# Kernel optimization log

Measured on AMD Instinct MI355X. Metric: run time of the kernel, lower is better.

Reference implementation:

```python
import jax, jax.numpy as jnp
import numpy as np

EPS = 1e-7
CAPS_N = 1152   # 32 maps * 6 * 6
CAPS1_DIM = 8
CAPS2_N = 10
CAPS2_DIM = 16


def squash(s, axis):
    sq = jnp.sum(jnp.square(s), axis=axis, keepdims=True)
    norm = jnp.sqrt(sq + EPS)
    return (sq / (1.0 + sq)) * (s / norm)


def _conv(x, k, b, stride):
    y = jax.lax.conv_general_dilated(x, k, (stride, stride), 'VALID',
                                     dimension_numbers=('NHWC', 'HWIO', 'NHWC'))
    return jax.nn.relu(y + b)


def setup_inputs() -> dict:
    key = jax.random.key(0)
    ks = jax.random.split(key, 8)
    B = 256
    return {
        'image': jax.random.uniform(ks[0], (B, 28, 28, 1), dtype=jnp.float32),
        'target': jax.random.randint(ks[1], (B,), 0, CAPS2_N),
        'conv1_w': jax.random.normal(ks[2], (9, 9, 1, 256), jnp.float32) * 0.05,
        'conv1_b': jnp.zeros((256,), jnp.float32),
        'conv2_w': jax.random.normal(ks[3], (9, 9, 256, 256), jnp.float32) * 0.02,
        'conv2_b': jnp.zeros((256,), jnp.float32),
        'W': jax.random.normal(ks[4], (1, CAPS_N, CAPS2_N, CAPS2_DIM, CAPS1_DIM), jnp.float32) * 0.1,
        'd1_w': jax.random.normal(ks[5], (CAPS2_N * CAPS2_DIM, 512), jnp.float32) * 0.05,
        'd1_b': jnp.zeros((512,), jnp.float32),
        'd2_w': jax.random.normal(ks[6], (512, 1024), jnp.float32) * 0.04,
        'd2_b': jnp.zeros((1024,), jnp.float32),
        'd3_w': jax.random.normal(ks[7], (1024, 784), jnp.float32) * 0.03,
        'd3_b': jnp.zeros((784,), jnp.float32),
    }


def reference(image, target, conv1_w, conv1_b, conv2_w, conv2_b, W,
              d1_w, d1_b, d2_w, d2_b, d3_w, d3_b):
    B = image.shape[0]
    h = _conv(image, conv1_w, conv1_b, 1)        # [B,20,20,256]
    h = _conv(h, conv2_w, conv2_b, 2)            # [B,6,6,256]
    pc = squash(h.reshape(B, CAPS_N, CAPS1_DIM), axis=-1)  # [B,1152,8]
    # u_hat[b,n,c,j] = sum_i W[0,n,c,j,i] * pc[b,n,i]  (avoids explicit tiling)
    u_hat = jnp.einsum('ncji,bni->bncj', W[0], pc)          # [B,1152,10,16]
    # round 1: softmax of zeros over the 10 digit caps == uniform 1/10
    s1 = jnp.sum(u_hat, axis=1) * (1.0 / CAPS2_N)           # [B,10,16]
    v1 = squash(s1, axis=-1)
    # agreement uv[b,n,c] = <u_hat[b,n,c,:], v1[b,c,:]>
    uv = jnp.einsum('bncj,bcj->bnc', u_hat, v1)             # [B,1152,10]
    # round 2
    c2 = jax.nn.softmax(uv, axis=2)
    s2 = jnp.einsum('bnc,bncj->bcj', c2, u_hat)             # [B,10,16]
    v2 = squash(s2, axis=-1)                                # [B,10,16]
    norm_v2 = jnp.sqrt(jnp.sum(jnp.square(v2), axis=-1, keepdims=True) + EPS)
    norm_v2 = norm_v2[:, None, :, :, None]                  # [B,1,10,1,1]
    y_pred = jnp.squeeze(jnp.argmax(norm_v2, axis=2), axis=(1, 2))  # [B,1]
    # training path: mask by target one-hot
    mask = jax.nn.one_hot(target, CAPS2_N, dtype=v2.dtype)  # [B,10]
    masked = v2 * mask[:, :, None]                          # [B,10,16]
    flat = masked.reshape(B, 1, CAPS2_N * CAPS2_DIM)        # [B,1,160]
    h1 = jax.nn.relu(flat @ d1_w + d1_b)
    h2 = jax.nn.relu(h1 @ d2_w + d2_b)
    dec = jax.nn.sigmoid(h2 @ d3_w + d3_b)                  # [B,1,784]
    return norm_v2, y_pred, dec
```

## Files before the change

kernel.cpp:

```cpp
#include <hip/hip_runtime.h>
#include <math.h>

#define EPS 1e-7f
#define IN1_ELEMS 26214400
#define BT_ELEMS  5308416

typedef float fvec4 __attribute__((ext_vector_type(4)));
typedef short short8 __attribute__((ext_vector_type(8)));
typedef _Float16 half8 __attribute__((ext_vector_type(8)));

__device__ inline unsigned short f2h(float f){
  _Float16 h = (_Float16)f;
  return __builtin_bit_cast(unsigned short, h);
}
__device__ inline float h2f(unsigned short u){
  return (float)__builtin_bit_cast(_Float16, u);
}
__device__ inline void async16(unsigned short* dst, const unsigned short* src){
  __builtin_amdgcn_global_load_lds((const __attribute__((address_space(1))) void*)src,
                                   (__attribute__((address_space(3))) void*)dst, 16, 0, 0);
}
__device__ inline fvec4 mfma_f16(short8 a, short8 b, fvec4 c){
  return __builtin_amdgcn_mfma_f32_16x16x32_f16(
      __builtin_bit_cast(half8, a), __builtin_bit_cast(half8, b), c, 0, 0, 0);
}

__global__ __launch_bounds__(256) void wt_kernel(const float* __restrict__ w2,
    unsigned short* __restrict__ BTh, unsigned short* __restrict__ BTl,
    float* __restrict__ c2out){
  __shared__ float tile[64][65];
  int t = threadIdx.x;
  int k0 = blockIdx.x * 64, oc0 = blockIdx.y * 64;
  int bid = blockIdx.y*324 + blockIdx.x;
  for (int g = bid*256 + t; g < 2359296; g += 1296*256) c2out[g] = 0.f;
  #pragma unroll
  for (int p = 0; p < 16; ++p){
    int f = p*256 + t;
    int kr = f >> 6, cc = f & 63;
    tile[kr][cc] = w2[(size_t)(k0 + kr)*256 + oc0 + cc];
  }
  __syncthreads();
  #pragma unroll
  for (int p = 0; p < 16; ++p){
    int f = p*256 + t;
    int ocr = f >> 6, kc = f & 63;
    float v = tile[kc][ocr] * 64.f;
    unsigned short h = f2h(v);
    size_t idx = (size_t)(oc0 + ocr)*20736 + k0 + kc;
    BTh[idx] = h;
    BTl[idx] = f2h(v - h2f(h));
  }
}

__global__ __launch_bounds__(256) void conv1_kernel(const float* __restrict__ img,
    const float* __restrict__ w1, const float* __restrict__ b1,
    unsigned short* __restrict__ outh){
  __shared__ float sim[252];
  int t = threadIdx.x;
  int oh = blockIdx.x, b = blockIdx.y;
  if (t < 252) sim[t] = img[((size_t)b*28 + oh + t/28)*28 + (t%28)];
  __syncthreads();
  float acc[20];
  #pragma unroll
  for (int i = 0; i < 20; ++i) acc[i] = 0.f;
  #pragma unroll
  for (int kh = 0; kh < 9; ++kh){
    float im[28];
    #pragma unroll
    for (int c = 0; c < 28; ++c) im[c] = sim[kh*28 + c];
    #pragma unroll
    for (int kw = 0; kw < 9; ++kw){
      float wv = w1[(kh*9 + kw)*256 + t];
      #pragma unroll
      for (int ow = 0; ow < 20; ++ow) acc[ow] = fmaf(im[ow + kw], wv, acc[ow]);
    }
  }
  float bv = b1[t];
  size_t base = ((size_t)(b*20 + oh))*20*256 + t;
  #pragma unroll
  for (int ow = 0; ow < 20; ++ow){
    float v = fmaxf(acc[ow] + bv, 0.f);
    outh[base + ow*256] = f2h(v * 0.015625f);
  }
}

__global__ __launch_bounds__(256) void conv2_mfma(const unsigned short* __restrict__ in1h,
    const unsigned short* __restrict__ BTh, float* __restrict__ out){
  __shared__ __align__(16) unsigned short lds[24576];
  const int t = threadIdx.x;
  const int lane = t & 63, w = t >> 6;
  const int m0 = blockIdx.y * 128, n0 = blockIdx.x * 128;
  const int rowA = t >> 2, q = (t & 3) ^ ((t >> 3) & 3);

  const unsigned short* aS[2];
  const unsigned short* bS[2];
  #pragma unroll
  for (int h = 0; h < 2; ++h){
    int m = m0 + h*64 + rowA;
    int bb = m / 36, s = m - bb*36, oh = s / 6, ow = s - oh*6;
    aS[h] = in1h + ((size_t)((bb*20 + 2*oh)*20 + 2*ow))*256 + q*8;
    int n = n0 + h*64 + rowA;
    bS[h] = BTh + (size_t)n*20736 + q*8;
  }

  const int r = lane & 15;
  const int p = (lane >> 4) ^ ((lane >> 1) & 3);
  int roA[4], roB[4];
  #pragma unroll
  for (int i=0;i<4;++i){
    roA[i] = ((w >> 1)*64 + i*16 + r)*32 + p*8;
    roB[i] = ((w & 1)*64  + i*16 + r)*32 + p*8;
  }

  fvec4 acc[4][4];
  #pragma unroll
  for (int i=0;i<4;++i)
    #pragma unroll
    for (int j=0;j<4;++j) acc[i][j] = (fvec4){0.f,0.f,0.f,0.f};

  const int ks0 = blockIdx.z * 81;

  #define STAGE(BUF, KS) do{                                            \
    int kk_ = (KS) >> 3, kh_ = kk_/9, kw_ = kk_ - kh_*9;                \
    int aoff_ = (kh_*20 + kw_)*256 + ((KS) & 7)*32;                     \
    int boff_ = (KS)*32;                                                \
    int base_ = (BUF)*12288;                                            \
    _Pragma("unroll")                                                   \
    for (int h_=0; h_<2; ++h_){                                         \
      async16(&lds[base_ +        h_*2048 + t*8], aS[h_] + aoff_);      \
      async16(&lds[base_ + 4096 + h_*2048 + t*8], bS[h_] + boff_);      \
      async16(&lds[base_ + 8192 + h_*2048 + t*8], bS[h_] + BT_ELEMS + boff_); \
    } }while(0)

  STAGE(0, ks0);
  int buf = 0;
  for (int it = 0; it < 81; ++it){
    __syncthreads();
    if (it < 80) STAGE(buf^1, ks0 + it + 1);
    int base = buf*12288;
    short8 af[4], bh[4], bl[4];
    #pragma unroll
    for (int i=0;i<4;++i){
      af[i] = *(const short8*)&lds[base + roA[i]];
      bh[i] = *(const short8*)&lds[base + 4096 + roB[i]];
      bl[i] = *(const short8*)&lds[base + 8192 + roB[i]];
    }
    #pragma unroll
    for (int i=0;i<4;++i)
      #pragma unroll
      for (int j=0;j<4;++j){
        acc[i][j] = mfma_f16(af[i], bh[j], acc[i][j]);
        acc[i][j] = mfma_f16(af[i], bl[j], acc[i][j]);
      }
    buf ^= 1;
  }

  const int qm = (w >> 1)*64, qn = (w & 1)*64;
  #pragma unroll
  for (int i=0;i<4;++i){
    int gm = m0 + qm + i*16 + ((lane >> 4) << 2);
    #pragma unroll
    for (int j=0;j<4;++j){
      int gn = n0 + qn + j*16 + (lane & 15);
      #pragma unroll
      for (int rr=0;rr<4;++rr)
        atomicAdd(&out[(size_t)(gm + rr)*256 + gn], acc[i][j][rr]);
    }
  }
}

__global__ __launch_bounds__(256) void squash_pc_kernel(const float* __restrict__ c2out,
    const float* __restrict__ b2, float* __restrict__ pc, float* __restrict__ s1s2){
  int g = blockIdx.x*256 + threadIdx.x;
  if (g < 81920) s1s2[g] = 0.f;
  const float* s = c2out + (size_t)g*8;
  int oc0 = (g & 31) * 8;
  float v[8], sq = 0.f;
  #pragma unroll
  for (int e=0;e<8;++e){ float x = fmaxf(s[e] + b2[oc0+e], 0.f); v[e] = x; sq += x*x; }
  float fac = sq / ((1.f + sq) * sqrtf(sq + EPS));
  float* o = pc + (size_t)g*8;
  #pragma unroll
  for (int e=0;e<8;++e) o[e] = v[e]*fac;
}

__global__ __launch_bounds__(256) void s1_producer(const float* __restrict__ pc,
    const float* __restrict__ Wm, float* __restrict__ s1){
  __shared__ float pcl[2048];
  int t = threadIdx.x;
  int n0 = blockIdx.x * 16, b0 = blockIdx.y * 16;
  #pragma unroll
  for (int p = 0; p < 8; ++p){
    int f = p*256 + t;
    int bl = f >> 7, rem = f & 127;
    pcl[f] = pc[((size_t)(b0 + bl)*1152 + n0)*8 + rem];
  }
  __syncthreads();
  for (int r = 0; r < 10; ++r){
    int item = r*256 + t;
    int bl = item / 160, cj = item - bl*160;
    float s1a = 0.f;
    const float* pb = &pcl[bl*128];
    #pragma unroll 4
    for (int nl = 0; nl < 16; ++nl){
      const float4* wp = (const float4*)&Wm[((size_t)(n0 + nl)*160 + cj)*8];
      float4 w0 = wp[0], w1 = wp[1];
      const float4* pp = (const float4*)&pb[nl*8];
      float4 p0 = pp[0], p1 = pp[1];
      s1a += w0.x*p0.x + w0.y*p0.y + w0.z*p0.z + w0.w*p0.w
           + w1.x*p1.x + w1.y*p1.y + w1.z*p1.z + w1.w*p1.w;
    }
    atomicAdd(&s1[(b0 + bl)*160 + cj], s1a);
  }
}

__global__ __launch_bounds__(320) void routing2(const float* __restrict__ pc,
    const float* __restrict__ Wm, const float* __restrict__ s1, float* __restrict__ s2){
  __shared__ float pcl[32][64];
  __shared__ float v1l[8][160];
  __shared__ float facl[80];
  __shared__ float c2l[32][10][8];
  const int t = threadIdx.x;
  const int n0 = blockIdx.x*32, b0 = blockIdx.y*8;

  for (int f = t; f < 2048; f += 320){
    int b = f >> 8, rem = f & 255;
    pcl[rem >> 3][b*8 + (rem & 7)] =
        pc[((size_t)(b0 + b)*1152 + n0 + (rem >> 3))*8 + (rem & 7)];
  }
  if (t < 80){
    int b = t/10, c = t - (t/10)*10;
    const float* s = s1 + (size_t)(b0 + b)*160 + c*16;
    float sq = 0.f;
    #pragma unroll
    for (int j=0;j<16;++j){ float v = s[j]*0.1f; sq += v*v; }
    facl[t] = 0.1f * sq / ((1.f + sq) * sqrtf(sq + EPS));
  }
  __syncthreads();
  for (int f = t; f < 1280; f += 320){
    int b = f / 160, cj = f - b*160;
    v1l[b][cj] = s1[(size_t)(b0 + b)*160 + cj] * facl[b*10 + (cj >> 4)];
  }
  __syncthreads();

  {
    const int nl = t / 10, c = t - (t/10)*10;
    float pcr[64];
    #pragma unroll
    for (int u = 0; u < 16; ++u) ((float4*)pcr)[u] = ((const float4*)&pcl[nl][0])[u];
    const float* wrow = Wm + ((size_t)(n0 + nl)*160 + c*16)*8;
    float uv[8];
    #pragma unroll
    for (int b=0;b<8;++b) uv[b] = 0.f;
    #pragma unroll
    for (int j = 0; j < 16; ++j){
      float4 w0 = ((const float4*)wrow)[j*2], w1 = ((const float4*)wrow)[j*2+1];
      #pragma unroll
      for (int b=0;b<8;++b){
        float tj = w0.x*pcr[b*8+0] + w0.y*pcr[b*8+1] + w0.z*pcr[b*8+2] + w0.w*pcr[b*8+3]
                 + w1.x*pcr[b*8+4] + w1.y*pcr[b*8+5] + w1.z*pcr[b*8+6] + w1.w*pcr[b*8+7];
        uv[b] = fmaf(tj, v1l[b][c*16 + j], uv[b]);
      }
    }
    #pragma unroll
    for (int b=0;b<8;++b) c2l[nl][c][b] = uv[b];
  }
  __syncthreads();

  if (t < 256){
    int snl = t >> 3, sb = t & 7;
    float mx = c2l[snl][0][sb];
    #pragma unroll
    for (int cc=1;cc<10;++cc) mx = fmaxf(mx, c2l[snl][cc][sb]);
    float e[10], sum = 0.f;
    #pragma unroll
    for (int cc=0;cc<10;++cc){ e[cc] = expf(c2l[snl][cc][sb] - mx); sum += e[cc]; }
    float inv = 1.f/sum;
    #pragma unroll
    for (int cc=0;cc<10;++cc) c2l[snl][cc][sb] = e[cc]*inv;
  }
  __syncthreads();

  {
    const int g = t / 160, cj = t - g*160;
    const int c = cj >> 4;
    float acc0 = 0.f, acc1 = 0.f, acc2 = 0.f, acc3 = 0.f;
    for (int nl = 0; nl < 32; ++nl){
      const float4* wp = (const float4*)&Wm[((size_t)(n0 + nl)*160 + cj)*8];
      float4 w0 = wp[0], w1 = wp[1];
      const float* pb = &pcl[nl][g*32];
      const float* cc = &c2l[nl][c][g*4];
      float4 p0, p1;
      p0 = ((const float4*)pb)[0]; p1 = ((const float4*)pb)[1];
      acc0 = fmaf(cc[0], w0.x*p0.x + w0.y*p0.y + w0.z*p0.z + w0.w*p0.w
                       + w1.x*p1.x + w1.y*p1.y + w1.z*p1.z + w1.w*p1.w, acc0);
      p0 = ((const float4*)pb)[2]; p1 = ((const float4*)pb)[3];
      acc1 = fmaf(cc[1], w0.x*p0.x + w0.y*p0.y + w0.z*p0.z + w0.w*p0.w
                       + w1.x*p1.x + w1.y*p1.y + w1.z*p1.z + w1.w*p1.w, acc1);
      p0 = ((const float4*)pb)[4]; p1 = ((const float4*)pb)[5];
      acc2 = fmaf(cc[2], w0.x*p0.x + w0.y*p0.y + w0.z*p0.z + w0.w*p0.w
                       + w1.x*p1.x + w1.y*p1.y + w1.z*p1.z + w1.w*p1.w, acc2);
      p0 = ((const float4*)pb)[6]; p1 = ((const float4*)pb)[7];
      acc3 = fmaf(cc[3], w0.x*p0.x + w0.y*p0.y + w0.z*p0.z + w0.w*p0.w
                       + w1.x*p1.x + w1.y*p1.y + w1.z*p1.z + w1.w*p1.w, acc3);
    }
    atomicAdd(&s2[(size_t)(b0 + g*4 + 0)*160 + cj], acc0);
    atomicAdd(&s2[(size_t)(b0 + g*4 + 1)*160 + cj], acc1);
    atomicAdd(&s2[(size_t)(b0 + g*4 + 2)*160 + cj], acc2);
    atomicAdd(&s2[(size_t)(b0 + g*4 + 3)*160 + cj], acc3);
  }
}

__global__ __launch_bounds__(64) void finalize_kernel(const float* __restrict__ s2,
    const int* __restrict__ target, float* __restrict__ out_norm,
    float* __restrict__ out_pred, float* __restrict__ masked){
  __shared__ float v2l[160];
  __shared__ float nrm[10];
  int b = blockIdx.x, t = threadIdx.x;
  if (t < 10){
    const float* s = s2 + b*160 + t*16;
    float x[16], sq = 0.f;
    #pragma unroll
    for (int j=0;j<16;++j){ x[j] = s[j]; sq += x[j]*x[j]; }
    float fac = sq / ((1.f + sq) * sqrtf(sq + EPS));
    float n2 = 0.f;
    #pragma unroll
    for (int j=0;j<16;++j){ float v = x[j]*fac; v2l[t*16+j] = v; n2 += v*v; }
    float nr = sqrtf(n2 + EPS);
    nrm[t] = nr;
    out_norm[b*10 + t] = nr;
  }
  __syncthreads();
  if (t == 0){
    int am = 0; float bv = nrm[0];
    #pragma unroll
    for (int c=1;c<10;++c) if (nrm[c] > bv){ bv = nrm[c]; am = c; }
    out_pred[b] = (float)am;
  }
  int tg = target[b];
  #pragma unroll
  for (int p = 0; p < 3; ++p){
    int cj = p*64 + t;
    if (cj < 160) masked[b*160 + cj] = ((cj >> 4) == tg) ? v2l[cj] : 0.f;
  }
}

__global__ __launch_bounds__(256) void dec_gemm(const float* __restrict__ A,
    const float* __restrict__ B, const float* __restrict__ bias, float* __restrict__ C,
    int K, int N, int act){
  int t = threadIdx.x;
  int n = blockIdx.x*64 + (t & 63);
  int m = blockIdx.y*4 + (t >> 6);
  if (n >= N) return;
  float acc = 0.f;
  const float* a = A + (size_t)m*K;
  const float* bp = B + n;
  #pragma unroll 8
  for (int k = 0; k < K; ++k) acc = fmaf(a[k], bp[(size_t)k*N], acc);
  acc += bias[n];
  if (act == 0) acc = fmaxf(acc, 0.f);
  else acc = 1.f/(1.f + expf(-acc));
  C[(size_t)m*N + n] = acc;
}

extern "C" void kernel_launch(void* const* d_in, const int* in_sizes, int n_in,
                              void* d_out, int out_size, void* d_ws, size_t ws_size,
                              hipStream_t stream) {
  const float* image   = (const float*)d_in[0];
  const int*   target  = (const int*)d_in[1];
  const float* conv1_w = (const float*)d_in[2];
  const float* conv1_b = (const float*)d_in[3];
  const float* conv2_w = (const float*)d_in[4];
  const float* conv2_b = (const float*)d_in[5];
  const float* Wm      = (const float*)d_in[6];
  const float* d1_w    = (const float*)d_in[7];
  const float* d1_b    = (const float*)d_in[8];
  const float* d2_w    = (const float*)d_in[9];
  const float* d2_b    = (const float*)d_in[10];
  const float* d3_w    = (const float*)d_in[11];
  const float* d3_b    = (const float*)d_in[12];

  char* ws = (char*)d_ws;
  unsigned short* in1h = (unsigned short*)(ws);
  unsigned short* BTh  = (unsigned short*)(ws + 52428800);
  float* c2out  = (float*)(ws + 73662464);
  float* pc     = (float*)(ws + 83099648);
  float* s1     = (float*)(ws + 92536832);
  float* s2     = (float*)(ws + 92700672);
  float* masked = (float*)(ws + 92864512);
  float* h1     = (float*)(ws + 93028352);
  float* h2     = (float*)(ws + 93552640);

  float* out_norm = (float*)d_out;
  float* out_pred = out_norm + 2560;
  float* dec      = out_norm + 2816;

  wt_kernel<<<dim3(324,4),256,0,stream>>>(conv2_w, BTh, BTh + BT_ELEMS, c2out);
  conv1_kernel<<<dim3(20,256),256,0,stream>>>(image, conv1_w, conv1_b, in1h);
  conv2_mfma<<<dim3(2,72,8),256,0,stream>>>(in1h, BTh, c2out);
  squash_pc_kernel<<<dim3(1152),256,0,stream>>>(c2out, conv2_b, pc, s1);
  s1_producer<<<dim3(72,16),256,0,stream>>>(pc, Wm, s1);
  routing2<<<dim3(36,32),320,0,stream>>>(pc, Wm, s1, s2);
  finalize_kernel<<<dim3(256),64,0,stream>>>(s2, target, out_norm, out_pred, masked);
  dec_gemm<<<dim3(8,64),256,0,stream>>>(masked, d1_w, d1_b, h1, 160, 512, 0);
  dec_gemm<<<dim3(16,64),256,0,stream>>>(h1, d2_w, d2_b, h2, 512, 1024, 0);
  dec_gemm<<<dim3(13,64),256,0,stream>>>(h2, d3_w, d3_b, dec, 1024, 784, 1);
}
```

Measured before the change: 633.4 us.

## Fuse prep kernels, squash into s1, final+dec1, and widen routing batch tile

Merges the weight transpose and conv1 into a single launch, folds the primary-capsule squash into the s1 producer, and fuses finalize with the first decoder layer by using only the target capsule's row of d1_w. Routing2 now handles 16 batches per block instead of 8, which halves the number of blocks and the reloads of W. The aim is to cut launch count and redundant global traffic. In exchange it adds register pressure and leaves fewer blocks in the routing kernel.

```diff
diff --git a/kernel.cpp b/kernel.cpp
--- a/kernel.cpp
+++ b/kernel.cpp
@@ -25,62 +25,64 @@
       __builtin_bit_cast(half8, a), __builtin_bit_cast(half8, b), c, 0, 0, 0);
 }
 
-__global__ __launch_bounds__(256) void wt_kernel(const float* __restrict__ w2,
+__global__ __launch_bounds__(256) void prep_kernel(const float* __restrict__ w2,
     unsigned short* __restrict__ BTh, unsigned short* __restrict__ BTl,
-    float* __restrict__ c2out){
-  __shared__ float tile[64][65];
-  int t = threadIdx.x;
-  int k0 = blockIdx.x * 64, oc0 = blockIdx.y * 64;
-  int bid = blockIdx.y*324 + blockIdx.x;
-  for (int g = bid*256 + t; g < 2359296; g += 1296*256) c2out[g] = 0.f;
-  #pragma unroll
-  for (int p = 0; p < 16; ++p){
-    int f = p*256 + t;
-    int kr = f >> 6, cc = f & 63;
-    tile[kr][cc] = w2[(size_t)(k0 + kr)*256 + oc0 + cc];
-  }
-  __syncthreads();
-  #pragma unroll
-  for (int p = 0; p < 16; ++p){
-    int f = p*256 + t;
-    int ocr = f >> 6, kc = f & 63;
-    float v = tile[kc][ocr] * 64.f;
-    unsigned short h = f2h(v);
-    size_t idx = (size_t)(oc0 + ocr)*20736 + k0 + kc;
-    BTh[idx] = h;
-    BTl[idx] = f2h(v - h2f(h));
-  }
-}
-
-__global__ __launch_bounds__(256) void conv1_kernel(const float* __restrict__ img,
-    const float* __restrict__ w1, const float* __restrict__ b1,
-    unsigned short* __restrict__ outh){
-  __shared__ float sim[252];
-  int t = threadIdx.x;
-  int oh = blockIdx.x, b = blockIdx.y;
-  if (t < 252) sim[t] = img[((size_t)b*28 + oh + t/28)*28 + (t%28)];
-  __syncthreads();
-  float acc[20];
-  #pragma unroll
-  for (int i = 0; i < 20; ++i) acc[i] = 0.f;
-  #pragma unroll
-  for (int kh = 0; kh < 9; ++kh){
-    float im[28];
-    #pragma unroll
-    for (int c = 0; c < 28; ++c) im[c] = sim[kh*28 + c];
-    #pragma unroll
-    for (int kw = 0; kw < 9; ++kw){
-      float wv = w1[(kh*9 + kw)*256 + t];
-      #pragma unroll
-      for (int ow = 0; ow < 20; ++ow) acc[ow] = fmaf(im[ow + kw], wv, acc[ow]);
-    }
-  }
-  float bv = b1[t];
-  size_t base = ((size_t)(b*20 + oh))*20*256 + t;
-  #pragma unroll
-  for (int ow = 0; ow < 20; ++ow){
-    float v = fmaxf(acc[ow] + bv, 0.f);
-    outh[base + ow*256] = f2h(v * 0.015625f);
+    float* __restrict__ c2out,
+    const float* __restrict__ img, const float* __restrict__ w1,
+    const float* __restrict__ b1, unsigned short* __restrict__ outh,
+    float* __restrict__ s1s2){
+  const int bid = blockIdx.x;
+  const int t = threadIdx.x;
+  if (bid < 1296){
+    __shared__ float tile[64][65];
+    int k0 = (bid % 324) * 64, oc0 = (bid / 324) * 64;
+    for (int g = bid*256 + t; g < 2359296; g += 1296*256) c2out[g] = 0.f;
+    #pragma unroll
+    for (int p = 0; p < 16; ++p){
+      int f = p*256 + t;
+      int kr = f >> 6, cc = f & 63;
+      tile[kr][cc] = w2[(size_t)(k0 + kr)*256 + oc0 + cc];
+    }
+    __syncthreads();
+    #pragma unroll
+    for (int p = 0; p < 16; ++p){
+      int f = p*256 + t;
+      int ocr = f >> 6, kc = f & 63;
+      float v = tile[kc][ocr] * 64.f;
+      unsigned short h = f2h(v);
+      size_t idx = (size_t)(oc0 + ocr)*20736 + k0 + kc;
+      BTh[idx] = h;
+      BTl[idx] = f2h(v - h2f(h));
+    }
+  } else {
+    const int cid = bid - 1296;
+    if (cid < 320) s1s2[cid*256 + t] = 0.f;
+    __shared__ float sim[252];
+    int oh = cid % 20, b = cid / 20;
+    if (t < 252) sim[t] = img[((size_t)b*28 + oh + t/28)*28 + (t%28)];
+    __syncthreads();
+    float acc[20];
+    #pragma unroll
+    for (int i = 0; i < 20; ++i) acc[i] = 0.f;
+    #pragma unroll
+    for (int kh = 0; kh < 9; ++kh){
+      float im[28];
+      #pragma unroll
+      for (int c = 0; c < 28; ++c) im[c] = sim[kh*28 + c];
+      #pragma unroll
+      for (int kw = 0; kw < 9; ++kw){
+        float wv = w1[(kh*9 + kw)*256 + t];
+        #pragma unroll
+        for (int ow = 0; ow < 20; ++ow) acc[ow] = fmaf(im[ow + kw], wv, acc[ow]);
+      }
+    }
+    float bv = b1[t];
+    size_t base = ((size_t)(b*20 + oh))*20*256 + t;
+    #pragma unroll
+    for (int ow = 0; ow < 20; ++ow){
+      float v = fmaxf(acc[ow] + bv, 0.f);
+      outh[base + ow*256] = f2h(v * 0.015625f);
+    }
   }
 }
 
@@ -169,31 +171,27 @@
   }
 }
 
-__global__ __launch_bounds__(256) void squash_pc_kernel(const float* __restrict__ c2out,
-    const float* __restrict__ b2, float* __restrict__ pc, float* __restrict__ s1s2){
-  int g = blockIdx.x*256 + threadIdx.x;
-  if (g < 81920) s1s2[g] = 0.f;
-  const float* s = c2out + (size_t)g*8;
-  int oc0 = (g & 31) * 8;
-  float v[8], sq = 0.f;
-  #pragma unroll
-  for (int e=0;e<8;++e){ float x = fmaxf(s[e] + b2[oc0+e], 0.f); v[e] = x; sq += x*x; }
-  float fac = sq / ((1.f + sq) * sqrtf(sq + EPS));
-  float* o = pc + (size_t)g*8;
-  #pragma unroll
-  for (int e=0;e<8;++e) o[e] = v[e]*fac;
-}
-
-__global__ __launch_bounds__(256) void s1_producer(const float* __restrict__ pc,
+__global__ __launch_bounds__(256) void s1pc_kernel(const float* __restrict__ c2out,
+    const float* __restrict__ b2, float* __restrict__ pc,
     const float* __restrict__ Wm, float* __restrict__ s1){
   __shared__ float pcl[2048];
   int t = threadIdx.x;
   int n0 = blockIdx.x * 16, b0 = blockIdx.y * 16;
-  #pragma unroll
-  for (int p = 0; p < 8; ++p){
-    int f = p*256 + t;
-    int bl = f >> 7, rem = f & 127;
-    pcl[f] = pc[((size_t)(b0 + bl)*1152 + n0)*8 + rem];
+  int pix = n0 >> 5, oc0 = (n0 & 31) * 8;
+  {
+    int bl = t >> 4, part = t & 15;
+    const float* s = c2out + ((size_t)((b0 + bl)*36 + pix))*256 + oc0 + part*8;
+    float v[8], sq = 0.f;
+    #pragma unroll
+    for (int e=0;e<8;++e){
+      float x = fmaxf(s[e] + b2[oc0 + part*8 + e], 0.f);
+      v[e] = x; sq += x*x;
+    }
+    float fac = sq / ((1.f + sq) * sqrtf(sq + EPS));
+    float* o = pc + ((size_t)(b0 + bl)*1152 + n0 + part)*8;
+    float* l = &pcl[(bl*16 + part)*8];
+    #pragma unroll
+    for (int e=0;e<8;++e){ float y = v[e]*fac; o[e] = y; l[e] = y; }
   }
   __syncthreads();
   for (int r = 0; r < 10; ++r){
@@ -216,19 +214,18 @@
 
 __global__ __launch_bounds__(320) void routing2(const float* __restrict__ pc,
     const float* __restrict__ Wm, const float* __restrict__ s1, float* __restrict__ s2){
-  __shared__ float pcl[32][64];
-  __shared__ float v1l[8][160];
-  __shared__ float facl[80];
-  __shared__ float c2l[32][10][8];
+  __shared__ float pcl[32][128];
+  __shared__ float v1l[16][160];
+  __shared__ float facl[160];
+  __shared__ float c2l[32][10][16];
   const int t = threadIdx.x;
-  const int n0 = blockIdx.x*32, b0 = blockIdx.y*8;
-
-  for (int f = t; f < 2048; f += 320){
-    int b = f >> 8, rem = f & 255;
-    pcl[rem >> 3][b*8 + (rem & 7)] =
-        pc[((size_t)(b0 + b)*1152 + n0 + (rem >> 3))*8 + (rem & 7)];
-  }
-  if (t < 80){
+  const int n0 = blockIdx.x*32, b0 = blockIdx.y*16;
+
+  for (int f = t; f < 4096; f += 320){
+    int nl = f >> 7, rem = f & 127;
+    pcl[nl][rem] = pc[((size_t)(b0 + (rem >> 3))*1152 + n0 + nl)*8 + (rem & 7)];
+  }
+  if (t < 160){
     int b = t/10, c = t - (t/10)*10;
     const float* s = s1 + (size_t)(b0 + b)*160 + c*16;
     float sq = 0.f;
@@ -237,7 +234,7 @@
     facl[t] = 0.1f * sq / ((1.f + sq) * sqrtf(sq + EPS));
   }
   __syncthreads();
-  for (int f = t; f < 1280; f += 320){
+  for (int f = t; f < 2560; f += 320){
     int b = f / 160, cj = f - b*160;
     v1l[b][cj] = s1[(size_t)(b0 + b)*160 + cj] * facl[b*10 + (cj >> 4)];
   }
@@ -245,30 +242,34 @@
 
   {
     const int nl = t / 10, c = t - (t/10)*10;
-    float pcr[64];
-    #pragma unroll
-    for (int u = 0; u < 16; ++u) ((float4*)pcr)[u] = ((const float4*)&pcl[nl][0])[u];
     const float* wrow = Wm + ((size_t)(n0 + nl)*160 + c*16)*8;
-    float uv[8];
-    #pragma unroll
-    for (int b=0;b<8;++b) uv[b] = 0.f;
-    #pragma unroll
-    for (int j = 0; j < 16; ++j){
-      float4 w0 = ((const float4*)wrow)[j*2], w1 = ((const float4*)wrow)[j*2+1];
-      #pragma unroll
-      for (int b=0;b<8;++b){
-        float tj = w0.x*pcr[b*8+0] + w0.y*pcr[b*8+1] + w0.z*pcr[b*8+2] + w0.w*pcr[b*8+3]
-                 + w1.x*pcr[b*8+4] + w1.y*pcr[b*8+5] + w1.z*pcr[b*8+6] + w1.w*pcr[b*8+7];
-        uv[b] = fmaf(tj, v1l[b][c*16 + j], uv[b]);
+    #pragma unroll
+    for (int g = 0; g < 2; ++g){
+      float pcr[64];
+      #pragma unroll
+      for (int u = 0; u < 16; ++u)
+        ((float4*)pcr)[u] = ((const float4*)&pcl[nl][g*64])[u];
+      float uv[8];
+      #pragma unroll
+      for (int b=0;b<8;++b) uv[b] = 0.f;
+      #pragma unroll
+      for (int j = 0; j < 16; ++j){
+        float4 w0 = ((const float4*)wrow)[j*2], w1 = ((const float4*)wrow)[j*2+1];
+        #pragma unroll
+        for (int b=0;b<8;++b){
+          float tj = w0.x*pcr[b*8+0] + w0.y*pcr[b*8+1] + w0.z*pcr[b*8+2] + w0.w*pcr[b*8+3]
+                   + w1.x*pcr[b*8+4] + w1.y*pcr[b*8+5] + w1.z*pcr[b*8+6] + w1.w*pcr[b*8+7];
+          uv[b] = fmaf(tj, v1l[g*8+b][c*16 + j], uv[b]);
+        }
       }
-    }
-    #pragma unroll
-    for (int b=0;b<8;++b) c2l[nl][c][b] = uv[b];
-  }
-  __syncthreads();
-
-  if (t < 256){
-    int snl = t >> 3, sb = t & 7;
+      #pragma unroll
+      for (int b=0;b<8;++b) c2l[nl][c][g*8+b] = uv[b];
+    }
+  }
+  __syncthreads();
+
+  for (int idx = t; idx < 512; idx += 320){
+    int snl = idx >> 4, sb = idx & 15;
     float mx = c2l[snl][0][sb];
     #pragma unroll
     for (int cc=1;cc<10;++cc) mx = fmaxf(mx, c2l[snl][cc][sb]);
@@ -282,41 +283,38 @@
   __syncthreads();
 
   {
-    const int g = t / 160, cj = t - g*160;
+    const int g = t / 160, cj = t - (t/160)*160;
     const int c = cj >> 4;
-    float acc0 = 0.f, acc1 = 0.f, acc2 = 0.f, acc3 = 0.f;
-    for (int nl = 0; nl < 32; ++nl){
+    float acc[16];
+    #pragma unroll
+    for (int b=0;b<16;++b) acc[b] = 0.f;
+    for (int nn = 0; nn < 16; ++nn){
+      int nl = g*16 + nn;
       const float4* wp = (const float4*)&Wm[((size_t)(n0 + nl)*160 + cj)*8];
       float4 w0 = wp[0], w1 = wp[1];
-      const float* pb = &pcl[nl][g*32];
-      const float* cc = &c2l[nl][c][g*4];
-      float4 p0, p1;
-      p0 = ((const float4*)pb)[0]; p1 = ((const float4*)pb)[1];
-      acc0 = fmaf(cc[0], w0.x*p0.x + w0.y*p0.y + w0.z*p0.z + w0.w*p0.w
-                       + w1.x*p1.x + w1.y*p1.y + w1.z*p1.z + w1.w*p1.w, acc0);
-      p0 = ((const float4*)pb)[2]; p1 = ((const float4*)pb)[3];
-      acc1 = fmaf(cc[1], w0.x*p0.x + w0.y*p0.y + w0.z*p0.z + w0.w*p0.w
-                       + w1.x*p1.x + w1.y*p1.y + w1.z*p1.z + w1.w*p1.w, acc1);
-      p0 = ((const float4*)pb)[4]; p1 = ((const float4*)pb)[5];
-      acc2 = fmaf(cc[2], w0.x*p0.x + w0.y*p0.y + w0.z*p0.z + w0.w*p0.w
-                       + w1.x*p1.x + w1.y*p1.y + w1.z*p1.z + w1.w*p1.w, acc2);
-      p0 = ((const float4*)pb)[6]; p1 = ((const float4*)pb)[7];
-      acc3 = fmaf(cc[3], w0.x*p0.x + w0.y*p0.y + w0.z*p0.z + w0.w*p0.w
-                       + w1.x*p1.x + w1.y*p1.y + w1.z*p1.z + w1.w*p1.w, acc3);
-    }
-    atomicAdd(&s2[(size_t)(b0 + g*4 + 0)*160 + cj], acc0);
-    atomicAdd(&s2[(size_t)(b0 + g*4 + 1)*160 + cj], acc1);
-    atomicAdd(&s2[(size_t)(b0 + g*4 + 2)*160 + cj], acc2);
-    atomicAdd(&s2[(size_t)(b0 + g*4 + 3)*160 + cj], acc3);
-  }
-}
-
-__global__ __launch_bounds__(64) void finalize_kernel(const float* __restrict__ s2,
-    const int* __restrict__ target, float* __restrict__ out_norm,
-    float* __restrict__ out_pred, float* __restrict__ masked){
-  __shared__ float v2l[160];
+      #pragma unroll
+      for (int b=0;b<16;++b){
+        const float4* pp = (const float4*)&pcl[nl][b*8];
+        float4 p0 = pp[0], p1 = pp[1];
+        float uh = w0.x*p0.x + w0.y*p0.y + w0.z*p0.z + w0.w*p0.w
+                 + w1.x*p1.x + w1.y*p1.y + w1.z*p1.z + w1.w*p1.w;
+        acc[b] = fmaf(c2l[nl][c][b], uh, acc[b]);
+      }
+    }
+    #pragma unroll
+    for (int b=0;b<16;++b)
+      atomicAdd(&s2[(size_t)(b0 + b)*160 + cj], acc[b]);
+  }
+}
+
+__global__ __launch_bounds__(128) void final_dec1(const float* __restrict__ s2,
+    const int* __restrict__ target, const float* __restrict__ d1w,
+    const float* __restrict__ d1b, float* __restrict__ out_norm,
+    float* __restrict__ out_pred, float* __restrict__ h1){
+  __shared__ float v2t[16];
   __shared__ float nrm[10];
   int b = blockIdx.x, t = threadIdx.x;
+  int tg = target[b];
   if (t < 10){
     const float* s = s2 + b*160 + t*16;
     float x[16], sq = 0.f;
@@ -325,7 +323,11 @@
     float fac = sq / ((1.f + sq) * sqrtf(sq + EPS));
     float n2 = 0.f;
     #pragma unroll
-    for (int j=0;j<16;++j){ float v = x[j]*fac; v2l[t*16+j] = v; n2 += v*v; }
+    for (int j=0;j<16;++j){
+      float v = x[j]*fac;
+      if (t == tg) v2t[j] = v;
+      n2 += v*v;
+    }
     float nr = sqrtf(n2 + EPS);
     nrm[t] = nr;
     out_norm[b*10 + t] = nr;
@@ -337,11 +339,16 @@
     for (int c=1;c<10;++c) if (nrm[c] > bv){ bv = nrm[c]; am = c; }
     out_pred[b] = (float)am;
   }
-  int tg = target[b];
-  #pragma unroll
-  for (int p = 0; p < 3; ++p){
-    int cj = p*64 + t;
-    if (cj < 160) masked[b*160 + cj] = ((cj >> 4) == tg) ? v2l[cj] : 0.f;
+  float v[16];
+  #pragma unroll
+  for (int j=0;j<16;++j) v[j] = v2t[j];
+  #pragma unroll
+  for (int rr = 0; rr < 4; ++rr){
+    int n = t + rr*128;
+    float acc = d1b[n];
+    #pragma unroll
+    for (int j=0;j<16;++j) acc = fmaf(v[j], d1w[(size_t)(tg*16 + j)*512 + n], acc);
+    h1[(size_t)b*512 + n] = fmaxf(acc, 0.f);
   }
 }
 
@@ -387,22 +394,19 @@
   float* pc     = (float*)(ws + 83099648);
   float* s1     = (float*)(ws + 92536832);
   float* s2     = (float*)(ws + 92700672);
-  float* masked = (float*)(ws + 92864512);
-  float* h1     = (float*)(ws + 93028352);
-  float* h2     = (float*)(ws + 93552640);
+  float* h1     = (float*)(ws + 92864512);
+  float* h2     = (float*)(ws + 93388800);
 
   float* out_norm = (float*)d_out;
   float* out_pred = out_norm + 2560;
   float* dec      = out_norm + 2816;
 
-  wt_kernel<<<dim3(324,4),256,0,stream>>>(conv2_w, BTh, BTh + BT_ELEMS, c2out);
-  conv1_kernel<<<dim3(20,256),256,0,stream>>>(image, conv1_w, conv1_b, in1h);
+  prep_kernel<<<dim3(6416),256,0,stream>>>(conv2_w, BTh, BTh + BT_ELEMS, c2out,
+                                           image, conv1_w, conv1_b, in1h, s1);
   conv2_mfma<<<dim3(2,72,8),256,0,stream>>>(in1h, BTh, c2out);
-  squash_pc_kernel<<<dim3(1152),256,0,stream>>>(c2out, conv2_b, pc, s1);
-  s1_producer<<<dim3(72,16),256,0,stream>>>(pc, Wm, s1);
-  routing2<<<dim3(36,32),320,0,stream>>>(pc, Wm, s1, s2);
-  finalize_kernel<<<dim3(256),64,0,stream>>>(s2, target, out_norm, out_pred, masked);
-  dec_gemm<<<dim3(8,64),256,0,stream>>>(masked, d1_w, d1_b, h1, 160, 512, 0);
+  s1pc_kernel<<<dim3(72,16),256,0,stream>>>(c2out, conv2_b, pc, Wm, s1);
+  routing2<<<dim3(36,16),320,0,stream>>>(pc, Wm, s1, s2);
+  final_dec1<<<dim3(256),128,0,stream>>>(s2, target, d1_w, d1_b, out_norm, out_pred, h1);
   dec_gemm<<<dim3(16,64),256,0,stream>>>(h1, d2_w, d2_b, h2, 512, 1024, 0);
   dec_gemm<<<dim3(13,64),256,0,stream>>>(h2, d3_w, d3_b, dec, 1024, 784, 1);
 }
```

Result: slower. 690.0 us (+8.9%).
